# Kernel tuning notes

Measured on AMD Instinct MI355X. Metric: run time of the kernel, lower is better.

Reference implementation:

```python
import jax, jax.numpy as jnp
import numpy as np

N_NODES = 100000
N_EDGES = 3200000
HIDDEN = 64
OUT = 1


def setup_inputs() -> dict:
    key = jax.random.key(0)
    k_z, k_e, k_w1, k_b1, k_w2, k_b2 = jax.random.split(key, 6)
    z = jax.random.normal(k_z, (N_NODES, HIDDEN), dtype=jnp.float32)
    edge_index = jax.random.randint(k_e, (2, N_EDGES), 0, N_NODES, dtype=jnp.int64)
    # torch Linear default init: U(-1/sqrt(fan_in), 1/sqrt(fan_in))
    lim1 = 1.0 / np.sqrt(2 * HIDDEN)
    lim2 = 1.0 / np.sqrt(HIDDEN)
    W1 = jax.random.uniform(k_w1, (2 * HIDDEN, HIDDEN), jnp.float32, -lim1, lim1)
    b1 = jax.random.uniform(k_b1, (HIDDEN,), jnp.float32, -lim1, lim1)
    W2 = jax.random.uniform(k_w2, (HIDDEN, OUT), jnp.float32, -lim2, lim2)
    b2 = jax.random.uniform(k_b2, (OUT,), jnp.float32, -lim2, lim2)
    return {"z": z, "edge_index": edge_index, "W1": W1, "b1": b1, "W2": W2, "b2": b2}


def reference(z, edge_index, W1, b1, W2, b2):
    row, col = edge_index[0], edge_index[1]
    # gather + concat: [E, 2*HIDDEN]
    h = jnp.concatenate([z[row], z[col]], axis=-1)
    h = jax.nn.relu(h @ W1 + b1)   # [E, HIDDEN]
    out = h @ W2 + b2              # [E, OUT]
    return out
```

## Files before the change

kernel.cpp:

```cpp
#include <hip/hip_runtime.h>
#include <hip/hip_bf16.h>

#define HID 64

typedef __attribute__((ext_vector_type(8))) short bf16x8;
typedef __attribute__((ext_vector_type(4))) float f32x4;

__device__ __forceinline__ unsigned short f2bf(float f) {
    unsigned int u = __float_as_uint(f);
    return (unsigned short)((u + 0x7fffu + ((u >> 16) & 1u)) >> 16);
}

__device__ __forceinline__ unsigned int pack2bf(float lo, float hi) {
    unsigned int ul = __float_as_uint(lo), uh = __float_as_uint(hi);
    unsigned int rl = (ul + 0x7fffu + ((ul >> 16) & 1u)) >> 16;
    unsigned int rh = (uh + 0x7fffu + ((uh >> 16) & 1u)) & 0xffff0000u;
    return rl | rh;
}

__global__ __launch_bounds__(256) void prep_weights(
    const float* __restrict__ W1, unsigned short* __restrict__ W1bt)
{
    const int t = blockIdx.x * 256 + threadIdx.x;
    const int c = t >> 6, k = t & 63;
    W1bt[t] = f2bf(W1[(((c >> 6) << 6) + k) * HID + (c & 63)]);
}

__global__ __launch_bounds__(256) void node_proj_mfma(
    const float* __restrict__ z, const unsigned short* __restrict__ W1bt,
    const float* __restrict__ b1,
    unsigned short* __restrict__ A, unsigned short* __restrict__ B,
    int n_tiles)
{
    const int tid  = blockIdx.x * 256 + threadIdx.x;
    const int lane = tid & 63;
    const int wv   = tid >> 6;
    const int nw   = (gridDim.x * 256) >> 6;
    const int q    = lane >> 4;
    const int r    = lane & 15;

    bf16x8 wf[8][2];
#pragma unroll
    for (int ct = 0; ct < 8; ++ct)
#pragma unroll
        for (int ks = 0; ks < 2; ++ks)
            wf[ct][ks] = *(const bf16x8*)(W1bt + (ct * 16 + r) * HID + ks * 32 + q * 8);

    float bias[4];
#pragma unroll
    for (int i = 0; i < 4; ++i) bias[i] = b1[i * 16 + r];

    for (int t = wv; t < n_tiles; t += nw) {
        const int rowb = t * 16;
        const float* zb = z + (size_t)(rowb + r) * HID;

        bf16x8 af[2];
#pragma unroll
        for (int ks = 0; ks < 2; ++ks) {
            const float4 f0 = *(const float4*)(zb + ks * 32 + q * 8);
            const float4 f1 = *(const float4*)(zb + ks * 32 + q * 8 + 4);
            unsigned int u[4];
            u[0] = pack2bf(f0.x, f0.y); u[1] = pack2bf(f0.z, f0.w);
            u[2] = pack2bf(f1.x, f1.y); u[3] = pack2bf(f1.z, f1.w);
            af[ks] = *(bf16x8*)u;
        }

#pragma unroll
        for (int ct = 0; ct < 8; ++ct) {
            f32x4 acc = {0.f, 0.f, 0.f, 0.f};
            acc = __builtin_amdgcn_mfma_f32_16x16x32_bf16(af[0], wf[ct][0], acc, 0, 0, 0);
            acc = __builtin_amdgcn_mfma_f32_16x16x32_bf16(af[1], wf[ct][1], acc, 0, 0, 0);
            const bool isB = (ct >= 4);
            const float bv = isB ? bias[ct & 3] : 0.0f;
            unsigned short* __restrict__ dst = isB ? B : A;
            const int colw = (ct & 3) * 16 + r;
#pragma unroll
            for (int j = 0; j < 4; ++j) {
                const int node = rowb + q * 4 + j;
                dst[(size_t)node * HID + colw] = f2bf(acc[j] + bv);
            }
        }
    }
}

__global__ __launch_bounds__(256) void edge_kernel(
    const int* __restrict__ row, const int* __restrict__ col,
    const unsigned short* __restrict__ A, const unsigned short* __restrict__ B,
    const float* __restrict__ W2, const float* __restrict__ b2,
    float* __restrict__ out, int E)
{
    const int tid    = blockIdx.x * blockDim.x + threadIdx.x;
    const int lane   = tid & 63;
    const int gwave  = tid >> 6;
    const int nwaves = (gridDim.x * blockDim.x) >> 6;
    const int sub    = lane >> 3;
    const int l8     = lane & 7;

    float w2r[8];
#pragma unroll
    for (int i = 0; i < 8; ++i) w2r[i] = W2[l8 * 8 + i];
    const float b2v = b2[0];

    const int nchunks = E >> 6;
    for (int ch = gwave; ch < nchunks; ch += nwaves) {
        const int ebase = ch << 6;
        const int r = row[ebase + lane];
        const int c = col[ebase + lane];

        uint4 av[8], bv[8];
#pragma unroll
        for (int g = 0; g < 8; ++g) {
            const int ri = __shfl(r, g * 8 + sub);
            const int ci = __shfl(c, g * 8 + sub);
            av[g] = *(const uint4*)(A + (size_t)ri * HID + l8 * 8);
            bv[g] = *(const uint4*)(B + (size_t)ci * HID + l8 * 8);
        }

#pragma unroll
        for (int g = 0; g < 8; ++g) {
            const unsigned int* au = (const unsigned int*)&av[g];
            const unsigned int* bu = (const unsigned int*)&bv[g];
            float acc = 0.f;
#pragma unroll
            for (int i = 0; i < 4; ++i) {
                float alo = __uint_as_float(au[i] << 16);
                float ahi = __uint_as_float(au[i] & 0xffff0000u);
                float blo = __uint_as_float(bu[i] << 16);
                float bhi = __uint_as_float(bu[i] & 0xffff0000u);
                acc = fmaf(fmaxf(alo + blo, 0.f), w2r[2 * i + 0], acc);
                acc = fmaf(fmaxf(ahi + bhi, 0.f), w2r[2 * i + 1], acc);
            }
            acc += __shfl_xor(acc, 4);
            acc += __shfl_xor(acc, 2);
            acc += __shfl_xor(acc, 1);
            if (l8 == 0) out[ebase + g * 8 + sub] = acc + b2v;
        }
    }
}

extern "C" void kernel_launch(void* const* d_in, const int* in_sizes, int n_in,
                              void* d_out, int out_size, void* d_ws, size_t ws_size,
                              hipStream_t stream) {
    const float* z  = (const float*)d_in[0];
    const int*   ei = (const int*)d_in[1];
    const float* W1 = (const float*)d_in[2];
    const float* b1 = (const float*)d_in[3];
    const float* W2 = (const float*)d_in[4];
    const float* b2 = (const float*)d_in[5];
    float* out = (float*)d_out;

    const int n_nodes = in_sizes[0] / HID;
    const int E       = in_sizes[1] / 2;
    const int* row = ei;
    const int* col = ei + E;

    unsigned short* A = (unsigned short*)d_ws;
    unsigned short* B = A + (size_t)n_nodes * HID;
    unsigned short* W1bt = B + (size_t)n_nodes * HID;

    prep_weights<<<32, 256, 0, stream>>>(W1, W1bt);
    node_proj_mfma<<<1024, 256, 0, stream>>>(z, W1bt, b1, A, B, n_nodes / 16);
    edge_kernel<<<2048, 256, 0, stream>>>(row, col, A, B, W2, b2, out, E);
}
```

Measured before the change: 206.3 us.

## Fuse weight prep into node projection with LDS staging of W1 and z

```diff
diff --git a/kernel.cpp b/kernel.cpp
--- a/kernel.cpp
+++ b/kernel.cpp
@@ -2,6 +2,8 @@
 #include <hip/hip_bf16.h>
 
 #define HID 64
+#define ZSTRIDE 68
+#define WSTRIDE 72
 
 typedef __attribute__((ext_vector_type(8))) short bf16x8;
 typedef __attribute__((ext_vector_type(4))) float f32x4;
@@ -18,67 +20,79 @@
     return rl | rh;
 }
 
-__global__ __launch_bounds__(256) void prep_weights(
-    const float* __restrict__ W1, unsigned short* __restrict__ W1bt)
-{
-    const int t = blockIdx.x * 256 + threadIdx.x;
-    const int c = t >> 6, k = t & 63;
-    W1bt[t] = f2bf(W1[(((c >> 6) << 6) + k) * HID + (c & 63)]);
-}
-
 __global__ __launch_bounds__(256) void node_proj_mfma(
-    const float* __restrict__ z, const unsigned short* __restrict__ W1bt,
+    const float* __restrict__ z, const float* __restrict__ W1,
     const float* __restrict__ b1,
     unsigned short* __restrict__ A, unsigned short* __restrict__ B,
-    int n_tiles)
+    int n_nodes)
 {
-    const int tid  = blockIdx.x * 256 + threadIdx.x;
-    const int lane = tid & 63;
-    const int wv   = tid >> 6;
-    const int nw   = (gridDim.x * 256) >> 6;
+    __shared__ alignas(16) float          zlds[64 * ZSTRIDE];
+    __shared__ alignas(16) unsigned short w1lds[128 * WSTRIDE];
+
+    const int t    = threadIdx.x;
+    const int lane = t & 63;
+    const int wv   = t >> 6;
     const int q    = lane >> 4;
     const int r    = lane & 15;
+    const int base = blockIdx.x * 64;
+
+#pragma unroll
+    for (int i = 0; i < 32; ++i) {
+        const int idx = t + i * 256;
+        const int kk  = idx >> 6;
+        const int j   = idx & 63;
+        const int c   = ((kk >> 6) << 6) | j;
+        w1lds[c * WSTRIDE + (kk & 63)] = f2bf(W1[idx]);
+    }
+
+#pragma unroll
+    for (int i = 0; i < 4; ++i) {
+        const int flat = t + i * 256;
+        const int row = flat >> 4, c4 = flat & 15;
+        int gr = base + row;
+        if (gr >= n_nodes) gr = n_nodes - 1;
+        *(float4*)(zlds + row * ZSTRIDE + c4 * 4) =
+            *(const float4*)(z + (size_t)gr * HID + c4 * 4);
+    }
+    __syncthreads();
 
     bf16x8 wf[8][2];
 #pragma unroll
     for (int ct = 0; ct < 8; ++ct)
 #pragma unroll
         for (int ks = 0; ks < 2; ++ks)
-            wf[ct][ks] = *(const bf16x8*)(W1bt + (ct * 16 + r) * HID + ks * 32 + q * 8);
+            wf[ct][ks] = *(const bf16x8*)(w1lds + (ct * 16 + r) * WSTRIDE + ks * 32 + q * 8);
+
+    bf16x8 af[2];
+#pragma unroll
+    for (int ks = 0; ks < 2; ++ks) {
+        const float* zp = zlds + (wv * 16 + r) * ZSTRIDE + ks * 32 + q * 8;
+        const float4 f0 = *(const float4*)zp;
+        const float4 f1 = *(const float4*)(zp + 4);
+        unsigned int u[4];
+        u[0] = pack2bf(f0.x, f0.y); u[1] = pack2bf(f0.z, f0.w);
+        u[2] = pack2bf(f1.x, f1.y); u[3] = pack2bf(f1.z, f1.w);
+        af[ks] = *(bf16x8*)u;
+    }
 
     float bias[4];
 #pragma unroll
     for (int i = 0; i < 4; ++i) bias[i] = b1[i * 16 + r];
 
-    for (int t = wv; t < n_tiles; t += nw) {
-        const int rowb = t * 16;
-        const float* zb = z + (size_t)(rowb + r) * HID;
-
-        bf16x8 af[2];
+    const int rowb = base + wv * 16;
 #pragma unroll
-        for (int ks = 0; ks < 2; ++ks) {
-            const float4 f0 = *(const float4*)(zb + ks * 32 + q * 8);
-            const float4 f1 = *(const float4*)(zb + ks * 32 + q * 8 + 4);
-            unsigned int u[4];
-            u[0] = pack2bf(f0.x, f0.y); u[1] = pack2bf(f0.z, f0.w);
-            u[2] = pack2bf(f1.x, f1.y); u[3] = pack2bf(f1.z, f1.w);
-            af[ks] = *(bf16x8*)u;
-        }
-
+    for (int ct = 0; ct < 8; ++ct) {
+        f32x4 acc = {0.f, 0.f, 0.f, 0.f};
+        acc = __builtin_amdgcn_mfma_f32_16x16x32_bf16(af[0], wf[ct][0], acc, 0, 0, 0);
+        acc = __builtin_amdgcn_mfma_f32_16x16x32_bf16(af[1], wf[ct][1], acc, 0, 0, 0);
+        const bool isB = (ct >= 4);
+        const float bv = isB ? bias[ct & 3] : 0.0f;
+        unsigned short* __restrict__ dst = isB ? B : A;
+        const int colw = (ct & 3) * 16 + r;
 #pragma unroll
-        for (int ct = 0; ct < 8; ++ct) {
-            f32x4 acc = {0.f, 0.f, 0.f, 0.f};
-            acc = __builtin_amdgcn_mfma_f32_16x16x32_bf16(af[0], wf[ct][0], acc, 0, 0, 0);
-            acc = __builtin_amdgcn_mfma_f32_16x16x32_bf16(af[1], wf[ct][1], acc, 0, 0, 0);
-            const bool isB = (ct >= 4);
-            const float bv = isB ? bias[ct & 3] : 0.0f;
-            unsigned short* __restrict__ dst = isB ? B : A;
-            const int colw = (ct & 3) * 16 + r;
-#pragma unroll
-            for (int j = 0; j < 4; ++j) {
-                const int node = rowb + q * 4 + j;
-                dst[(size_t)node * HID + colw] = f2bf(acc[j] + bv);
-            }
+        for (int j = 0; j < 4; ++j) {
+            const int node = rowb + q * 4 + j;
+            if (node < n_nodes) dst[(size_t)node * HID + colw] = f2bf(acc[j] + bv);
         }
     }
 }
@@ -156,9 +170,8 @@
 
     unsigned short* A = (unsigned short*)d_ws;
     unsigned short* B = A + (size_t)n_nodes * HID;
-    unsigned short* W1bt = B + (size_t)n_nodes * HID;
 
-    prep_weights<<<32, 256, 0, stream>>>(W1, W1bt);
-    node_proj_mfma<<<1024, 256, 0, stream>>>(z, W1bt, b1, A, B, n_nodes / 16);
+    const int nblocks = (n_nodes + 63) / 64;
+    node_proj_mfma<<<nblocks, 256, 0, stream>>>(z, W1, b1, A, B, n_nodes);
     edge_kernel<<<2048, 256, 0, stream>>>(row, col, A, B, W2, b2, out, E);
 }
```

Result: faster. 199.5 us (-3.3%).

## Stage node projection through LDS for coalesced stores; split edge kernel in two

Applied to the files above, without the earlier changes.

```diff
diff --git a/kernel.cpp b/kernel.cpp
--- a/kernel.cpp
+++ b/kernel.cpp
@@ -2,6 +2,7 @@
 #include <hip/hip_bf16.h>
 
 #define HID 64
+#define SST 132
 
 typedef __attribute__((ext_vector_type(8))) short bf16x8;
 typedef __attribute__((ext_vector_type(4))) float f32x4;
@@ -30,14 +31,16 @@
     const float* __restrict__ z, const unsigned short* __restrict__ W1bt,
     const float* __restrict__ b1,
     unsigned short* __restrict__ A, unsigned short* __restrict__ B,
-    int n_tiles)
+    int n_nodes)
 {
-    const int tid  = blockIdx.x * 256 + threadIdx.x;
-    const int lane = tid & 63;
-    const int wv   = tid >> 6;
-    const int nw   = (gridDim.x * 256) >> 6;
+    __shared__ alignas(16) unsigned short slds[64 * SST];
+
+    const int t    = threadIdx.x;
+    const int lane = t & 63;
+    const int wv   = t >> 6;
     const int q    = lane >> 4;
     const int r    = lane & 15;
+    const int base = blockIdx.x * 64;
 
     bf16x8 wf[8][2];
 #pragma unroll
@@ -50,35 +53,49 @@
 #pragma unroll
     for (int i = 0; i < 4; ++i) bias[i] = b1[i * 16 + r];
 
-    for (int t = wv; t < n_tiles; t += nw) {
-        const int rowb = t * 16;
-        const float* zb = z + (size_t)(rowb + r) * HID;
-
-        bf16x8 af[2];
+    const int rowb = base + wv * 16;
+    int zrow = rowb + r;
+    if (zrow >= n_nodes) zrow = n_nodes - 1;
+    const float* zb = z + (size_t)zrow * HID;
+    bf16x8 af[2];
 #pragma unroll
-        for (int ks = 0; ks < 2; ++ks) {
-            const float4 f0 = *(const float4*)(zb + ks * 32 + q * 8);
-            const float4 f1 = *(const float4*)(zb + ks * 32 + q * 8 + 4);
-            unsigned int u[4];
-            u[0] = pack2bf(f0.x, f0.y); u[1] = pack2bf(f0.z, f0.w);
-            u[2] = pack2bf(f1.x, f1.y); u[3] = pack2bf(f1.z, f1.w);
-            af[ks] = *(bf16x8*)u;
-        }
+    for (int ks = 0; ks < 2; ++ks) {
+        const float4 f0 = *(const float4*)(zb + ks * 32 + q * 8);
+        const float4 f1 = *(const float4*)(zb + ks * 32 + q * 8 + 4);
+        unsigned int u[4];
+        u[0] = pack2bf(f0.x, f0.y); u[1] = pack2bf(f0.z, f0.w);
+        u[2] = pack2bf(f1.x, f1.y); u[3] = pack2bf(f1.z, f1.w);
+        af[ks] = *(bf16x8*)u;
+    }
 
 #pragma unroll
-        for (int ct = 0; ct < 8; ++ct) {
-            f32x4 acc = {0.f, 0.f, 0.f, 0.f};
-            acc = __builtin_amdgcn_mfma_f32_16x16x32_bf16(af[0], wf[ct][0], acc, 0, 0, 0);
-            acc = __builtin_amdgcn_mfma_f32_16x16x32_bf16(af[1], wf[ct][1], acc, 0, 0, 0);
-            const bool isB = (ct >= 4);
-            const float bv = isB ? bias[ct & 3] : 0.0f;
-            unsigned short* __restrict__ dst = isB ? B : A;
-            const int colw = (ct & 3) * 16 + r;
+    for (int ct = 0; ct < 8; ++ct) {
+        f32x4 acc = {0.f, 0.f, 0.f, 0.f};
+        acc = __builtin_amdgcn_mfma_f32_16x16x32_bf16(af[0], wf[ct][0], acc, 0, 0, 0);
+        acc = __builtin_amdgcn_mfma_f32_16x16x32_bf16(af[1], wf[ct][1], acc, 0, 0, 0);
+        const float bv = (ct >= 4) ? bias[ct & 3] : 0.0f;
+        const int c = ct * 16 + r;
 #pragma unroll
-            for (int j = 0; j < 4; ++j) {
-                const int node = rowb + q * 4 + j;
-                dst[(size_t)node * HID + colw] = f2bf(acc[j] + bv);
-            }
+        for (int j = 0; j < 4; ++j) {
+            const int nl = wv * 16 + q * 4 + j;
+            slds[nl * SST + c] = f2bf(acc[j] + bv);
+        }
+    }
+    __syncthreads();
+
+#pragma unroll
+    for (int rep = 0; rep < 2; ++rep) {
+        const int i   = t + rep * 256;
+        const int nl  = i >> 3, seg = i & 7;
+        const int ng  = base + nl;
+        if (ng < n_nodes) {
+            const uint2* pa = (const uint2*)(slds + nl * SST + seg * 8);
+            const uint2* pb = (const uint2*)(slds + nl * SST + 64 + seg * 8);
+            uint4 va, vb;
+            va.x = pa[0].x; va.y = pa[0].y; va.z = pa[1].x; va.w = pa[1].y;
+            vb.x = pb[0].x; vb.y = pb[0].y; vb.z = pb[1].x; vb.w = pb[1].y;
+            *(uint4*)(A + (size_t)ng * HID + seg * 8) = va;
+            *(uint4*)(B + (size_t)ng * HID + seg * 8) = vb;
         }
     }
 }
@@ -87,7 +104,7 @@
     const int* __restrict__ row, const int* __restrict__ col,
     const unsigned short* __restrict__ A, const unsigned short* __restrict__ B,
     const float* __restrict__ W2, const float* __restrict__ b2,
-    float* __restrict__ out, int E)
+    float* __restrict__ out, int cbegin, int cend)
 {
     const int tid    = blockIdx.x * blockDim.x + threadIdx.x;
     const int lane   = tid & 63;
@@ -101,8 +118,7 @@
     for (int i = 0; i < 8; ++i) w2r[i] = W2[l8 * 8 + i];
     const float b2v = b2[0];
 
-    const int nchunks = E >> 6;
-    for (int ch = gwave; ch < nchunks; ch += nwaves) {
+    for (int ch = cbegin + gwave; ch < cend; ch += nwaves) {
         const int ebase = ch << 6;
         const int r = row[ebase + lane];
         const int c = col[ebase + lane];
@@ -159,6 +175,11 @@
     unsigned short* W1bt = B + (size_t)n_nodes * HID;
 
     prep_weights<<<32, 256, 0, stream>>>(W1, W1bt);
-    node_proj_mfma<<<1024, 256, 0, stream>>>(z, W1bt, b1, A, B, n_nodes / 16);
-    edge_kernel<<<2048, 256, 0, stream>>>(row, col, A, B, W2, b2, out, E);
+    const int nblocks = (n_nodes + 63) / 64;
+    node_proj_mfma<<<nblocks, 256, 0, stream>>>(z, W1bt, b1, A, B, n_nodes);
+
+    const int nchunks = E >> 6;
+    const int half = nchunks / 2;
+    edge_kernel<<<2048, 256, 0, stream>>>(row, col, A, B, W2, b2, out, 0, half);
+    edge_kernel<<<2048, 256, 0, stream>>>(row, col, A, B, W2, b2, out, half, nchunks);
 }
```

Measured after the change: 209.9 us. About the same (+1.8%).

## Compute edge MLP per edge with MFMA on gathered bf16 z instead of node projections

Applied to the files above, without the earlier changes.

```diff
diff --git a/kernel.cpp b/kernel.cpp
--- a/kernel.cpp
+++ b/kernel.cpp
@@ -1,7 +1,7 @@
 #include <hip/hip_runtime.h>
-#include <hip/hip_bf16.h>
 
 #define HID 64
+#define WST 72
 
 typedef __attribute__((ext_vector_type(8))) short bf16x8;
 typedef __attribute__((ext_vector_type(4))) float f32x4;
@@ -18,122 +18,114 @@
     return rl | rh;
 }
 
-__global__ __launch_bounds__(256) void prep_weights(
-    const float* __restrict__ W1, unsigned short* __restrict__ W1bt)
+__global__ __launch_bounds__(256) void zconv_kernel(
+    const float* __restrict__ z, uint4* __restrict__ zb, int n4)
 {
     const int t = blockIdx.x * 256 + threadIdx.x;
-    const int c = t >> 6, k = t & 63;
-    W1bt[t] = f2bf(W1[(((c >> 6) << 6) + k) * HID + (c & 63)]);
+    if (t < n4) {
+        const float4 f0 = ((const float4*)z)[2 * t];
+        const float4 f1 = ((const float4*)z)[2 * t + 1];
+        uint4 u;
+        u.x = pack2bf(f0.x, f0.y); u.y = pack2bf(f0.z, f0.w);
+        u.z = pack2bf(f1.x, f1.y); u.w = pack2bf(f1.z, f1.w);
+        zb[t] = u;
+    }
 }
 
-__global__ __launch_bounds__(256) void node_proj_mfma(
-    const float* __restrict__ z, const unsigned short* __restrict__ W1bt,
-    const float* __restrict__ b1,
-    unsigned short* __restrict__ A, unsigned short* __restrict__ B,
-    int n_tiles)
+__global__ __launch_bounds__(256) void edge_mfma_kernel(
+    const int* __restrict__ row, const int* __restrict__ col,
+    const unsigned short* __restrict__ zb,
+    const float* __restrict__ W1, const float* __restrict__ b1,
+    const float* __restrict__ W2, const float* __restrict__ b2,
+    float* __restrict__ out, int nchunks)
 {
-    const int tid  = blockIdx.x * 256 + threadIdx.x;
-    const int lane = tid & 63;
-    const int wv   = tid >> 6;
-    const int nw   = (gridDim.x * 256) >> 6;
+    __shared__ alignas(16) unsigned short wlds[128 * WST];
+
+    const int t    = threadIdx.x;
+    const int lane = t & 63;
     const int q    = lane >> 4;
     const int r    = lane & 15;
 
-    bf16x8 wf[8][2];
 #pragma unroll
-    for (int ct = 0; ct < 8; ++ct)
+    for (int i = 0; i < 8; ++i) {
+        const int f  = t + i * 256;
+        const int kk = f >> 4;
+        const int j4 = f & 15;
+        const int cb = (kk & 64) + j4 * 4;
+        const int k  = kk & 63;
+        const float4 v = ((const float4*)W1)[f];
+        wlds[(cb + 0) * WST + k] = f2bf(v.x);
+        wlds[(cb + 1) * WST + k] = f2bf(v.y);
+        wlds[(cb + 2) * WST + k] = f2bf(v.z);
+        wlds[(cb + 3) * WST + k] = f2bf(v.w);
+    }
+    __syncthreads();
+
+    float w2r[4], bias[4];
 #pragma unroll
-        for (int ks = 0; ks < 2; ++ks)
-            wf[ct][ks] = *(const bf16x8*)(W1bt + (ct * 16 + r) * HID + ks * 32 + q * 8);
+    for (int nt = 0; nt < 4; ++nt) {
+        w2r[nt]  = W2[nt * 16 + r];
+        bias[nt] = b1[nt * 16 + r];
+    }
+    const float b2v = b2[0];
 
-    float bias[4];
+    const int wid = (blockIdx.x * 256 + t) >> 6;
+    const int nw  = (gridDim.x * 256) >> 6;
+
+    for (int ch = wid; ch < nchunks; ch += nw) {
+        const int ebase = ch << 6;
+        const int ridx = row[ebase + lane];
+        const int cidx = col[ebase + lane];
+
+        uint4 gr[4][2], gc[4][2];
 #pragma unroll
-    for (int i = 0; i < 4; ++i) bias[i] = b1[i * 16 + r];
+        for (int mt = 0; mt < 4; ++mt) {
+            const int er = __shfl(ridx, mt * 16 + r);
+            const int ec = __shfl(cidx, mt * 16 + r);
+            const unsigned short* pr = zb + (size_t)er * HID + q * 8;
+            const unsigned short* pc = zb + (size_t)ec * HID + q * 8;
+            gr[mt][0] = *(const uint4*)pr;
+            gr[mt][1] = *(const uint4*)(pr + 32);
+            gc[mt][0] = *(const uint4*)pc;
+            gc[mt][1] = *(const uint4*)(pc + 32);
+        }
 
-    for (int t = wv; t < n_tiles; t += nw) {
-        const int rowb = t * 16;
-        const float* zb = z + (size_t)(rowb + r) * HID;
-
-        bf16x8 af[2];
+        f32x4 part[4] = {{0,0,0,0},{0,0,0,0},{0,0,0,0},{0,0,0,0}};
 #pragma unroll
-        for (int ks = 0; ks < 2; ++ks) {
-            const float4 f0 = *(const float4*)(zb + ks * 32 + q * 8);
-            const float4 f1 = *(const float4*)(zb + ks * 32 + q * 8 + 4);
-            unsigned int u[4];
-            u[0] = pack2bf(f0.x, f0.y); u[1] = pack2bf(f0.z, f0.w);
-            u[2] = pack2bf(f1.x, f1.y); u[3] = pack2bf(f1.z, f1.w);
-            af[ks] = *(bf16x8*)u;
+        for (int nt = 0; nt < 4; ++nt) {
+            const unsigned short* wp = wlds + (nt * 16 + r) * WST + q * 8;
+            const bf16x8 wa0 = *(const bf16x8*)wp;
+            const bf16x8 wa1 = *(const bf16x8*)(wp + 32);
+            const bf16x8 wb0 = *(const bf16x8*)(wp + 64 * WST);
+            const bf16x8 wb1 = *(const bf16x8*)(wp + 64 * WST + 32);
+#pragma unroll
+            for (int mt = 0; mt < 4; ++mt) {
+                f32x4 acc = {0.f, 0.f, 0.f, 0.f};
+                acc = __builtin_amdgcn_mfma_f32_16x16x32_bf16(*(const bf16x8*)&gr[mt][0], wa0, acc, 0, 0, 0);
+                acc = __builtin_amdgcn_mfma_f32_16x16x32_bf16(*(const bf16x8*)&gr[mt][1], wa1, acc, 0, 0, 0);
+                acc = __builtin_amdgcn_mfma_f32_16x16x32_bf16(*(const bf16x8*)&gc[mt][0], wb0, acc, 0, 0, 0);
+                acc = __builtin_amdgcn_mfma_f32_16x16x32_bf16(*(const bf16x8*)&gc[mt][1], wb1, acc, 0, 0, 0);
+#pragma unroll
+                for (int j = 0; j < 4; ++j)
+                    part[mt][j] = fmaf(fmaxf(acc[j] + bias[nt], 0.f), w2r[nt], part[mt][j]);
+            }
         }
 
 #pragma unroll
-        for (int ct = 0; ct < 8; ++ct) {
-            f32x4 acc = {0.f, 0.f, 0.f, 0.f};
-            acc = __builtin_amdgcn_mfma_f32_16x16x32_bf16(af[0], wf[ct][0], acc, 0, 0, 0);
-            acc = __builtin_amdgcn_mfma_f32_16x16x32_bf16(af[1], wf[ct][1], acc, 0, 0, 0);
-            const bool isB = (ct >= 4);
-            const float bv = isB ? bias[ct & 3] : 0.0f;
-            unsigned short* __restrict__ dst = isB ? B : A;
-            const int colw = (ct & 3) * 16 + r;
+        for (int mt = 0; mt < 4; ++mt) {
+            float4 o;
+            float* po = (float*)&o;
 #pragma unroll
             for (int j = 0; j < 4; ++j) {
-                const int node = rowb + q * 4 + j;
-                dst[(size_t)node * HID + colw] = f2bf(acc[j] + bv);
+                float p = part[mt][j];
+                p += __shfl_xor(p, 1);
+                p += __shfl_xor(p, 2);
+                p += __shfl_xor(p, 4);
+                p += __shfl_xor(p, 8);
+                po[j] = p + b2v;
             }
-        }
-    }
-}
-
-__global__ __launch_bounds__(256) void edge_kernel(
-    const int* __restrict__ row, const int* __restrict__ col,
-    const unsigned short* __restrict__ A, const unsigned short* __restrict__ B,
-    const float* __restrict__ W2, const float* __restrict__ b2,
-    float* __restrict__ out, int E)
-{
-    const int tid    = blockIdx.x * blockDim.x + threadIdx.x;
-    const int lane   = tid & 63;
-    const int gwave  = tid >> 6;
-    const int nwaves = (gridDim.x * blockDim.x) >> 6;
-    const int sub    = lane >> 3;
-    const int l8     = lane & 7;
-
-    float w2r[8];
-#pragma unroll
-    for (int i = 0; i < 8; ++i) w2r[i] = W2[l8 * 8 + i];
-    const float b2v = b2[0];
-
-    const int nchunks = E >> 6;
-    for (int ch = gwave; ch < nchunks; ch += nwaves) {
-        const int ebase = ch << 6;
-        const int r = row[ebase + lane];
-        const int c = col[ebase + lane];
-
-        uint4 av[8], bv[8];
-#pragma unroll
-        for (int g = 0; g < 8; ++g) {
-            const int ri = __shfl(r, g * 8 + sub);
-            const int ci = __shfl(c, g * 8 + sub);
-            av[g] = *(const uint4*)(A + (size_t)ri * HID + l8 * 8);
-            bv[g] = *(const uint4*)(B + (size_t)ci * HID + l8 * 8);
-        }
-
-#pragma unroll
-        for (int g = 0; g < 8; ++g) {
-            const unsigned int* au = (const unsigned int*)&av[g];
-            const unsigned int* bu = (const unsigned int*)&bv[g];
-            float acc = 0.f;
-#pragma unroll
-            for (int i = 0; i < 4; ++i) {
-                float alo = __uint_as_float(au[i] << 16);
-                float ahi = __uint_as_float(au[i] & 0xffff0000u);
-                float blo = __uint_as_float(bu[i] << 16);
-                float bhi = __uint_as_float(bu[i] & 0xffff0000u);
-                acc = fmaf(fmaxf(alo + blo, 0.f), w2r[2 * i + 0], acc);
-                acc = fmaf(fmaxf(ahi + bhi, 0.f), w2r[2 * i + 1], acc);
-            }
-            acc += __shfl_xor(acc, 4);
-            acc += __shfl_xor(acc, 2);
-            acc += __shfl_xor(acc, 1);
-            if (l8 == 0) out[ebase + g * 8 + sub] = acc + b2v;
+            if (r == 0)
+                *(float4*)(out + ebase + mt * 16 + q * 4) = o;
         }
     }
 }
@@ -154,11 +146,12 @@
     const int* row = ei;
     const int* col = ei + E;
 
-    unsigned short* A = (unsigned short*)d_ws;
-    unsigned short* B = A + (size_t)n_nodes * HID;
-    unsigned short* W1bt = B + (size_t)n_nodes * HID;
+    unsigned short* zb = (unsigned short*)d_ws;
 
-    prep_weights<<<32, 256, 0, stream>>>(W1, W1bt);
-    node_proj_mfma<<<1024, 256, 0, stream>>>(z, W1bt, b1, A, B, n_nodes / 16);
-    edge_kernel<<<2048, 256, 0, stream>>>(row, col, A, B, W2, b2, out, E);
+    const int n4 = n_nodes * HID / 8;
+    zconv_kernel<<<(n4 + 255) / 256, 256, 0, stream>>>(z, (uint4*)zb, n4);
+
+    const int nchunks = E >> 6;
+    edge_mfma_kernel<<<2048, 256, 0, stream>>>(row, col, zb, W1, b1, W2, b2,
+                                               out, nchunks);
 }
```

After: 217.2 us. 5.3% more time.
